# Kernel optimization log

Measured on AMD Instinct MI355X. Metric: run time of the kernel, lower is better.

Reference implementation:

```python
import jax, jax.numpy as jnp
import numpy as np

B, T, D = 2, 1024, 1024
H, HKV = 16, 8
HD = D // H           # 64
NREP = H // HKV       # 2
NLAYERS = 3
MAXKV = T * NLAYERS   # 3072
EPS = 1e-5


def setup_inputs() -> dict:
    key = jax.random.key(0)
    ks = jax.random.split(key, 8)
    # rotary tables over full accumulated-KV range
    inv_freq = 1.0 / (10000.0 ** (jnp.arange(0, HD, 2, dtype=jnp.float32) / HD))  # (HD/2,)
    t = jnp.arange(MAXKV, dtype=jnp.float32)
    freqs = jnp.outer(t, inv_freq)  # (MAXKV, HD/2)
    return {
        "x": jax.random.normal(ks[0], (B, T, D), jnp.float32),
        "cos": jnp.cos(freqs),
        "sin": jnp.sin(freqs),
        "q_w": jax.random.normal(ks[1], (NLAYERS, D, D), jnp.float32) * 0.02,
        "k_w": jax.random.normal(ks[2], (NLAYERS, D // NREP, D), jnp.float32) * 0.02,
        "v_w": jax.random.normal(ks[3], (NLAYERS, D // NREP, D), jnp.float32) * 0.02,
        "ln_w": jnp.ones((NLAYERS, D), jnp.float32),
        "lam": jax.random.normal(ks[4], (NLAYERS,), jnp.float32) * 0.1,
        "out_w": jax.random.normal(ks[5], (D, D), jnp.float32) * 0.02,
        "final_ln_w": jnp.ones((D,), jnp.float32),
        "alpha": jnp.ones((1,), jnp.float32),
    }


def rmsnorm(x, w):
    return x * jax.lax.rsqrt(jnp.mean(x * x, axis=-1, keepdims=True) + EPS) * w


def rope(x, cos, sin):
    # x: (B, L, h, HD); cos/sin: (MAXKV, HD/2); flash_attn non-interleaved rotary
    L = x.shape[1]
    c = jnp.concatenate([cos[:L], cos[:L]], axis=-1)[None, :, None, :]
    s = jnp.concatenate([sin[:L], sin[:L]], axis=-1)[None, :, None, :]
    x1, x2 = jnp.split(x, 2, axis=-1)
    rot = jnp.concatenate([-x2, x1], axis=-1)
    return x * c + rot * s


def reference(x, cos, sin, q_w, k_w, v_w, ln_w, lam, out_w, final_ln_w, alpha):
    scale = HD ** -0.5
    # lambda weights: layernorm over sigmoid of the 3 scalars (biased var, eps=1e-5)
    s = jax.nn.sigmoid(lam)
    lw = (s - s.mean()) * jax.lax.rsqrt(s.var() + EPS)
    qidx = jnp.arange(T)
    k_list, v_list = [], []
    acc = jnp.zeros_like(x)
    for i in range(NLAYERS):
        q = (x @ q_w[i].T).reshape(B, T, H, HD)
        k = (x @ k_w[i].T).reshape(B, T, HKV, HD)
        v = (x @ v_w[i].T).reshape(B, T, HKV, HD)
        k_list.append(k)
        v_list.append(v)
        K = jnp.concatenate(k_list, axis=1)  # (B, L, HKV, HD), L=(i+1)*T
        V = jnp.concatenate(v_list, axis=1)
        L = K.shape[1]
        qr = rope(q, cos, sin)
        Kr = rope(K, cos, sin)  # whole buffer re-rotated each layer, as in original
        Kr = jnp.repeat(Kr, NREP, axis=2)  # GQA expand
        Vr = jnp.repeat(V, NREP, axis=2)
        scores = jnp.einsum('bqhd,bkhd->bhqk', qr, Kr) * scale
        # flash_attn causal=True with kv_len > q_len aligns bottom-right
        mask = jnp.arange(L)[None, :] <= (qidx + (L - T))[:, None]
        scores = jnp.where(mask[None, None], scores, -jnp.inf)
        attn = jax.nn.softmax(scores, axis=-1)
        o = jnp.einsum('bhqk,bkhd->bqhd', attn, Vr).reshape(B, T, D)
        acc = acc + rmsnorm(o, ln_w[i]) * lw[i]
    out = rmsnorm(acc + alpha * x, final_ln_w)
    return out @ out_w.T
```

## Files before the change

### kernel.cpp

```cpp
#include <hip/hip_runtime.h>
#include <type_traits>
#include <utility>

typedef unsigned short u16;
typedef unsigned int u32;
typedef short short8 __attribute__((ext_vector_type(8)));
typedef short s16x4 __attribute__((ext_vector_type(4)));
typedef __bf16 bf16x8 __attribute__((ext_vector_type(8)));
typedef float floatx4 __attribute__((ext_vector_type(4)));

template <typename V, typename = void> struct MfmaTakes : std::false_type {};
template <typename V>
struct MfmaTakes<V, std::void_t<decltype(__builtin_amdgcn_mfma_f32_16x16x32_bf16(
    std::declval<V>(), std::declval<V>(), std::declval<floatx4>(), 0, 0, 0))>>
    : std::true_type {};

template <typename V>
__device__ __forceinline__ floatx4 mfma_impl(V a, V b, floatx4 c, std::true_type) {
  return __builtin_amdgcn_mfma_f32_16x16x32_bf16(a, b, c, 0, 0, 0);
}
template <typename V>
__device__ __forceinline__ floatx4 mfma_impl(V a, V b, floatx4 c, std::false_type) {
  return __builtin_amdgcn_mfma_f32_16x16x32_bf16(
      __builtin_bit_cast(bf16x8, a), __builtin_bit_cast(bf16x8, b), c, 0, 0, 0);
}
__device__ __forceinline__ floatx4 MFMA16(short8 a, short8 b, floatx4 c) {
  return mfma_impl<short8>(a, b, c, MfmaTakes<short8>{});
}

__device__ __forceinline__ floatx4 MFMAK16(s16x4 a, s16x4 b, floatx4 c) {
  return __builtin_amdgcn_mfma_f32_16x16x16bf16_1k(a, b, c, 0, 0, 0);
}

#if defined(__has_builtin)
#if __has_builtin(__builtin_amdgcn_exp2f)
#define EXP2(x) __builtin_amdgcn_exp2f(x)
#else
#define EXP2(x) exp2f(x)
#endif
#else
#define EXP2(x) exp2f(x)
#endif

__device__ __forceinline__ u16 f2bf(float f) {
  union { float f; unsigned u; } x; x.f = f;
  unsigned r = (x.u + 0x7fffu + ((x.u >> 16) & 1u)) >> 16;
  return (u16)r;
}
__device__ __forceinline__ float bf2f(u16 v) {
  union { unsigned u; float f; } x; x.u = ((unsigned)v) << 16; return x.f;
}
__device__ __forceinline__ u32 packbf(float lo, float hi) {
  return (__float_as_uint(hi) & 0xffff0000u) | (__float_as_uint(lo) >> 16);
}
__device__ __forceinline__ u32 pack2bf(float lo, float hi) {
  return ((u32)f2bf(hi) << 16) | (u32)f2bf(lo);
}

#if defined(__has_builtin)
#if __has_builtin(__builtin_amdgcn_global_load_lds)
#define HAS_GLLDS 1
#endif
#endif
__device__ __forceinline__ void stage16(const u16* g, u16* lbase, int lane) {
#ifdef HAS_GLLDS
  __builtin_amdgcn_global_load_lds(
      (__attribute__((address_space(1))) void*)(g),
      (__attribute__((address_space(3))) void*)(lbase), 16, 0, 0);
#else
  *(uint4*)(lbase + lane * 8) = *(const uint4*)g;
#endif
}

#define QSCALE 0.18033688011112042f

__global__ __launch_bounds__(256) void prep_kernel(
    const float* __restrict__ x, const float* __restrict__ qw,
    const float* __restrict__ kw, const float* __restrict__ vw,
    const float* __restrict__ outw, const float* __restrict__ lam,
    u16* __restrict__ xb, u16* __restrict__ wcat, u16* __restrict__ outwb,
    float* __restrict__ lwbuf) {
  size_t gid = (size_t)blockIdx.x * 256 + threadIdx.x;
  if (gid == 0) {
    float s0 = 1.f / (1.f + expf(-lam[0]));
    float s1 = 1.f / (1.f + expf(-lam[1]));
    float s2 = 1.f / (1.f + expf(-lam[2]));
    float mean = (s0 + s1 + s2) * (1.f / 3.f);
    float d0 = s0 - mean, d1 = s1 - mean, d2 = s2 - mean;
    float var = (d0 * d0 + d1 * d1 + d2 * d2) * (1.f / 3.f);
    float r = rsqrtf(var + 1e-5f);
    lwbuf[0] = d0 * r; lwbuf[1] = d1 * r; lwbuf[2] = d2 * r;
  }
  if (gid < 524288) {
    float4 v = ((const float4*)x)[gid];
    ushort4 o; o.x = f2bf(v.x); o.y = f2bf(v.y); o.z = f2bf(v.z); o.w = f2bf(v.w);
    ((ushort4*)xb)[gid] = o;
    return;
  }
  size_t g2 = gid - 524288;
  if (g2 < 1572864) {
    int col4 = (int)(g2 & 255);
    int n = (int)(g2 >> 8);
    int layer = n >> 11, r = n & 2047;
    const float* srcrow;
    if (r < 1024) srcrow = qw + ((size_t)(layer * 1024 + r) << 10);
    else if (r < 1536) srcrow = kw + ((size_t)(layer * 512 + (r - 1024)) << 10);
    else srcrow = vw + ((size_t)(layer * 512 + (r - 1536)) << 10);
    float4 v = ((const float4*)srcrow)[col4];
    ushort4 o; o.x = f2bf(v.x); o.y = f2bf(v.y); o.z = f2bf(v.z); o.w = f2bf(v.w);
    ((ushort4*)wcat)[g2] = o;
    return;
  }
  size_t g3 = g2 - 1572864;
  if (g3 < 262144) {
    float4 v = ((const float4*)outw)[g3];
    ushort4 o; o.x = f2bf(v.x); o.y = f2bf(v.y); o.z = f2bf(v.z); o.w = f2bf(v.w);
    ((ushort4*)outwb)[g3] = o;
  }
}

__global__ __launch_bounds__(256) void gemm_qkv(
    const u16* __restrict__ A, const u16* __restrict__ Bw,
    const float* __restrict__ cosb, const float* __restrict__ sinb,
    u16* __restrict__ qr, u16* __restrict__ kr, u16* __restrict__ vt) {
  __shared__ u16 As[128][64];
  __shared__ u16 Bs[128][64];
  const unsigned flat = blockIdx.x;
  const int bm = (flat >> 3) & 15;
  const int bn = ((flat >> 7) << 3) + (flat & 7);
  const int tid = threadIdx.x;
  const int wave = tid >> 6, lane = tid & 63;
  const int quad = lane >> 4, l16 = lane & 15;
  const int wm = wave & 1, wn = wave >> 1;
  const int srow = lane >> 3, skc = (lane & 7) * 8;
  floatx4 acc[4][4];
#pragma unroll
  for (int i = 0; i < 4; i++)
#pragma unroll
    for (int j = 0; j < 4; j++) { acc[i][j][0] = 0.f; acc[i][j][1] = 0.f; acc[i][j][2] = 0.f; acc[i][j][3] = 0.f; }
  const u16* Abase = A + (size_t)(bm * 128) * 1024;
  const u16* Bbase = Bw + (size_t)(bn * 128) * 1024;
  for (int k0 = 0; k0 < 1024; k0 += 64) {
    __syncthreads();
#pragma unroll
    for (int i = 0; i < 4; i++) {
      int ch = wave * 4 + i;
      stage16(Abase + (size_t)(ch * 8 + srow) * 1024 + k0 + skc, &As[ch * 8][0], lane);
      stage16(Bbase + (size_t)(ch * 8 + srow) * 1024 + k0 + skc, &Bs[ch * 8][0], lane);
    }
    __syncthreads();
#pragma unroll
    for (int kf = 0; kf < 2; kf++) {
      short8 af[4], bf[4];
#pragma unroll
      for (int mi = 0; mi < 4; mi++)
        af[mi] = *(const short8*)(&As[wm * 64 + mi * 16 + l16][kf * 32 + quad * 8]);
#pragma unroll
      for (int ni = 0; ni < 4; ni++)
        bf[ni] = *(const short8*)(&Bs[wn * 64 + ni * 16 + l16][kf * 32 + quad * 8]);
#pragma unroll
      for (int mi = 0; mi < 4; mi++)
#pragma unroll
        for (int ni = 0; ni < 4; ni++)
          acc[mi][ni] = MFMA16(af[mi], bf[ni], acc[mi][ni]);
    }
  }
  const int f0 = bn * 128 + wn * 64;
  const int lay = f0 >> 11;
  const int r0 = f0 & 2047;
  const int mrow0 = bm * 128 + wm * 64;
  if (r0 < 1024) {
    const int h = r0 >> 6;
#pragma unroll
    for (int mi = 0; mi < 4; mi++)
#pragma unroll
      for (int rr = 0; rr < 4; rr++) {
        int m = mrow0 + mi * 16 + quad * 4 + rr;
        int b = m >> 10, t = m & 1023;
        const float* cp = cosb + (size_t)t * 32;
        const float* sp = sinb + (size_t)t * 32;
        float c0 = cp[l16], s0 = sp[l16];
        float c1 = cp[16 + l16], s1 = sp[16 + l16];
        float x10 = acc[mi][0][rr], x20 = acc[mi][2][rr];
        float x11 = acc[mi][1][rr], x21 = acc[mi][3][rr];
        u16* row = qr + ((((size_t)lay * 2 + b) * 16 + h) * 1024 + t) * 64;
        row[l16]      = f2bf((x10 * c0 - x20 * s0) * QSCALE);
        row[16 + l16] = f2bf((x11 * c1 - x21 * s1) * QSCALE);
        row[32 + l16] = f2bf((x20 * c0 + x10 * s0) * QSCALE);
        row[48 + l16] = f2bf((x21 * c1 + x11 * s1) * QSCALE);
      }
  } else if (r0 < 1536) {
    const int hk = (r0 - 1024) >> 6;
#pragma unroll
    for (int mi = 0; mi < 4; mi++)
#pragma unroll
      for (int rr = 0; rr < 4; rr++) {
        int m = mrow0 + mi * 16 + quad * 4 + rr;
        int b = m >> 10, t = m & 1023;
        int pos = lay * 1024 + t;
        const float* cp = cosb + (size_t)pos * 32;
        const float* sp = sinb + (size_t)pos * 32;
        float c0 = cp[l16], s0 = sp[l16];
        float c1 = cp[16 + l16], s1 = sp[16 + l16];
        float x10 = acc[mi][0][rr], x20 = acc[mi][2][rr];
        float x11 = acc[mi][1][rr], x21 = acc[mi][3][rr];
        u16* row = kr + (((size_t)(b * 8 + hk)) * 3072 + pos) * 64;
        row[l16]      = f2bf(x10 * c0 - x20 * s0);
        row[16 + l16] = f2bf(x11 * c1 - x21 * s1);
        row[32 + l16] = f2bf(x20 * c0 + x10 * s0);
        row[48 + l16] = f2bf(x21 * c1 + x11 * s1);
      }
  } else {
    const int hv = (r0 - 1536) >> 6;
#pragma unroll
    for (int mi = 0; mi < 4; mi++) {
      int m0 = mrow0 + mi * 16 + quad * 4;
      int b = m0 >> 10;
      int pos0 = lay * 1024 + (m0 & 1023);
      u16* colbase = vt + ((size_t)(b * 8 + hv) * 64) * 3072 + pos0;
#pragma unroll
      for (int ni = 0; ni < 4; ni++) {
        int d = ni * 16 + l16;
        uint2 st;
        st.x = pack2bf(acc[mi][ni][0], acc[mi][ni][1]);
        st.y = pack2bf(acc[mi][ni][2], acc[mi][ni][3]);
        *(uint2*)(colbase + (size_t)d * 3072) = st;
      }
    }
  }
}

__global__ __launch_bounds__(256) void gemm_bt(
    const u16* __restrict__ A, const u16* __restrict__ Bw,
    float* __restrict__ C, int N, int K) {
  __shared__ u16 As[64][72];
  __shared__ u16 Bs[64][72];
  const int bm = blockIdx.x, bn = blockIdx.y;
  const int tid = threadIdx.x;
  const int wave = tid >> 6, lane = tid & 63;
  const int quad = lane >> 4, l16 = lane & 15;
  const int lr = tid >> 2, lc = (tid & 3) << 4;
  floatx4 acc[4];
#pragma unroll
  for (int i = 0; i < 4; i++) { acc[i][0] = 0.f; acc[i][1] = 0.f; acc[i][2] = 0.f; acc[i][3] = 0.f; }
  const u16* Arow = A + (size_t)(bm * 64 + lr) * K;
  const u16* Brow = Bw + (size_t)(bn * 64 + lr) * K;
  for (int k0 = 0; k0 < K; k0 += 64) {
    __syncthreads();
    *(uint4*)(&As[lr][lc])     = *(const uint4*)(Arow + k0 + lc);
    *(uint4*)(&As[lr][lc + 8]) = *(const uint4*)(Arow + k0 + lc + 8);
    *(uint4*)(&Bs[lr][lc])     = *(const uint4*)(Brow + k0 + lc);
    *(uint4*)(&Bs[lr][lc + 8]) = *(const uint4*)(Brow + k0 + lc + 8);
    __syncthreads();
    const int mrow = wave * 16 + l16;
    short8 a0 = *(const short8*)(&As[mrow][quad * 8]);
    short8 a1 = *(const short8*)(&As[mrow][32 + quad * 8]);
#pragma unroll
    for (int ns = 0; ns < 4; ns++) {
      short8 b0 = *(const short8*)(&Bs[ns * 16 + l16][quad * 8]);
      short8 b1 = *(const short8*)(&Bs[ns * 16 + l16][32 + quad * 8]);
      acc[ns] = MFMA16(a0, b0, acc[ns]);
      acc[ns] = MFMA16(a1, b1, acc[ns]);
    }
  }
#pragma unroll
  for (int ns = 0; ns < 4; ns++)
#pragma unroll
    for (int r = 0; r < 4; r++) {
      int row = bm * 64 + wave * 16 + quad * 4 + r;
      int col = bn * 64 + ns * 16 + l16;
      C[(size_t)row * N + col] = acc[ns][r];
    }
}

__global__ __launch_bounds__(256) void attn_v7(
    const u16* __restrict__ qr, const u16* __restrict__ kr,
    const u16* __restrict__ vt, u16* __restrict__ obS,
    float* __restrict__ lbufp) {
  __shared__ __align__(16) u16 Kt[2][32][72];
  __shared__ __align__(16) u16 Vtt[2][64][40];
  __shared__ __align__(16) u16 Pw[4][16][40];
  const unsigned flat = blockIdx.x;
  const int xcd = (int)(flat & 7);
  const int m = (int)(flat >> 3);
  const int qtile = m / 24;
  const int gidx = m - qtile * 24;
  const int bhz = gidx * 8 + xcd;
  const int z = bhz >> 5;
  const int bh = bhz & 31;
  const int lay = (z == 5) ? 0 : ((z == 0 || z == 4) ? 1 : 2);
  const int n = lay * 32 + qtile * 4 + 4;
  int kt0, kt1;
  if (lay == 0) { kt0 = 0; kt1 = n; }
  else if (lay == 1) { int hf = n >> 1; kt0 = (z == 0) ? 0 : hf; kt1 = (z == 0) ? hf : n; }
  else {
    int t1 = n / 3, t2 = (2 * n) / 3;
    kt0 = (z == 1) ? 0 : ((z == 2) ? t1 : t2);
    kt1 = (z == 1) ? t1 : ((z == 2) ? t2 : n);
  }
  const int maskkt = lay * 32 + qtile * 4;
  const int b = bh >> 4, h = bh & 15, hk = h >> 1;
  const int tid = threadIdx.x, wave = tid >> 6, lane = tid & 63;
  const int quad = lane >> 4, l16 = lane & 15;
  const int qeffbase = lay * 1024 + qtile * 128 + wave * 32;
  const u16* qpb = qr + ((((size_t)lay * 2 + b) * 16 + h) * 1024
                         + qtile * 128 + wave * 32 + l16) * 64 + quad * 8;
  short8 qf[2][2];
  qf[0][0] = *(const short8*)(qpb);
  qf[0][1] = *(const short8*)(qpb + 32);
  qf[1][0] = *(const short8*)(qpb + 1024);
  qf[1][1] = *(const short8*)(qpb + 1056);
  const s16x4 ones4 = {16256, 16256, 16256, 16256};
  floatx4 oacc[2][4];
#pragma unroll
  for (int nt = 0; nt < 2; nt++)
#pragma unroll
    for (int dt = 0; dt < 4; dt++) { oacc[nt][dt][0] = 0.f; oacc[nt][dt][1] = 0.f; oacc[nt][dt][2] = 0.f; oacc[nt][dt][3] = 0.f; }
  floatx4 lacc[2];
  lacc[0][0] = 0.f; lacc[0][1] = 0.f; lacc[0][2] = 0.f; lacc[0][3] = 0.f;
  lacc[1] = lacc[0];
  const int ksr = tid >> 3, ksc = (tid & 7) * 8;
  const int vdr = tid >> 2, vdc = (tid & 3) * 8;
  const u16* kp = kr + ((size_t)(b * 8 + hk) * 3072 + kt0 * 32 + ksr) * 64 + ksc;
  const u16* vp = vt + ((size_t)(b * 8 + hk) * 64 + vdr) * 3072 + kt0 * 32 + vdc;
  uint4 kA = *(const uint4*)kp;
  uint4 vA = *(const uint4*)vp;
  *(uint4*)(&Kt[0][ksr][ksc])  = kA;
  *(uint4*)(&Vtt[0][vdr][vdc]) = vA;
  kp += 2048; vp += 32;
  if (kt0 + 1 < kt1) { kA = *(const uint4*)kp; vA = *(const uint4*)vp; }
  for (int kt = kt0; kt < kt1; kt++) {
    const int p = (kt - kt0) & 1;
    __syncthreads();
    if (kt + 1 < kt1) {
      *(uint4*)(&Kt[p ^ 1][ksr][ksc])  = kA;
      *(uint4*)(&Vtt[p ^ 1][vdr][vdc]) = vA;
      kp += 2048; vp += 32;
      if (kt + 2 < kt1) { kA = *(const uint4*)kp; vA = *(const uint4*)vp; }
    }
    const bool needmask = (kt >= maskkt);
    uint2 pk[2][2];
#pragma unroll
    for (int mt = 0; mt < 2; mt++) {
      short8 kfa = *(const short8*)(&Kt[p][mt * 16 + l16][quad * 8]);
      short8 kfb = *(const short8*)(&Kt[p][mt * 16 + l16][32 + quad * 8]);
      const int keyb = kt * 32 + mt * 16 + quad * 4;
#pragma unroll
      for (int nt = 0; nt < 2; nt++) {
        floatx4 s; s[0] = 0.f; s[1] = 0.f; s[2] = 0.f; s[3] = 0.f;
        s = MFMA16(kfa, qf[nt][0], s);
        s = MFMA16(kfb, qf[nt][1], s);
        float p0 = EXP2(s[0]), p1 = EXP2(s[1]);
        float p2 = EXP2(s[2]), p3 = EXP2(s[3]);
        if (needmask) {
          int qpos = qeffbase + nt * 16 + l16;
          if (keyb + 0 > qpos) p0 = 0.f;
          if (keyb + 1 > qpos) p1 = 0.f;
          if (keyb + 2 > qpos) p2 = 0.f;
          if (keyb + 3 > qpos) p3 = 0.f;
        }
        pk[mt][nt].x = packbf(p0, p1);
        pk[mt][nt].y = packbf(p2, p3);
      }
    }
    s16x4 vfr[2][4];
#pragma unroll
    for (int dt = 0; dt < 4; dt++) {
      vfr[0][dt] = *(const s16x4*)(&Vtt[p][dt * 16 + l16][quad * 4]);
      vfr[1][dt] = *(const s16x4*)(&Vtt[p][dt * 16 + l16][16 + quad * 4]);
    }
#pragma unroll
    for (int nt = 0; nt < 2; nt++) {
      s16x4 p0f = __builtin_bit_cast(s16x4, pk[0][nt]);
      s16x4 p1f = __builtin_bit_cast(s16x4, pk[1][nt]);
      lacc[nt] = MFMAK16(ones4, p0f, lacc[nt]);
      lacc[nt] = MFMAK16(ones4, p1f, lacc[nt]);
#pragma unroll
      for (int dt = 0; dt < 4; dt++) {
        oacc[nt][dt] = MFMAK16(vfr[0][dt], p0f, oacc[nt][dt]);
        oacc[nt][dt] = MFMAK16(vfr[1][dt], p1f, oacc[nt][dt]);
      }
    }
  }
  float* Pf = (float*)(&Pw[wave][0][0]);
  const int tt = lane >> 2, dd = (lane & 3) << 2;
#pragma unroll
  for (int nt = 0; nt < 2; nt++) {
    int t = qtile * 128 + wave * 32 + nt * 16 + l16;
    if (quad == 0)
      lbufp[((size_t)z * 2048 + b * 1024 + t) * 16 + h] = lacc[nt][0];
    int t2 = qtile * 128 + wave * 32 + nt * 16 + tt;
    u16* orow = obS + ((size_t)(z * 2 + b) * 1024 + t2) * 1024 + h * 64 + dd;
#pragma unroll
    for (int dt = 0; dt < 4; dt++) {
      *(floatx4*)(&Pf[l16 * 20 + quad * 4]) = oacc[nt][dt];
      floatx4 val = *(const floatx4*)(&Pf[tt * 20 + dd]);
      uint2 st; st.x = pack2bf(val[0], val[1]); st.y = pack2bf(val[2], val[3]);
      *(uint2*)(orow + dt * 16) = st;
    }
  }
}

__device__ __forceinline__ float block_sum(float v, float* red) {
  v += __shfl_xor(v, 32); v += __shfl_xor(v, 16); v += __shfl_xor(v, 8);
  v += __shfl_xor(v, 4);  v += __shfl_xor(v, 2);  v += __shfl_xor(v, 1);
  __syncthreads();
  if ((threadIdx.x & 63) == 0) red[threadIdx.x >> 6] = v;
  __syncthreads();
  return red[0] + red[1] + red[2] + red[3];
}

__global__ __launch_bounds__(256) void fused_norm(
    const u16* __restrict__ obS, const float* __restrict__ lbufp,
    const float* __restrict__ x, const float* __restrict__ lnw,
    const float* __restrict__ lwbuf, const float* __restrict__ flnw,
    const float* __restrict__ alphap, u16* __restrict__ y) {
  __shared__ float red[4];
  const int row = blockIdx.x, tid = threadIdx.x;
  float a[4] = {0.f, 0.f, 0.f, 0.f};
  const int nsl[3] = {1, 2, 3};
  const int sl[3][3] = {{5, 0, 0}, {0, 4, 0}, {1, 2, 3}};
#pragma unroll
  for (int l = 0; l < 3; l++) {
    float o0 = 0.f, o1 = 0.f, o2 = 0.f, o3 = 0.f, ls = 0.f;
#pragma unroll
    for (int si = 0; si < 3; si++) {
      if (si >= nsl[l]) break;
      int z = sl[l][si];
      uint2 v = ((const uint2*)(obS + ((size_t)z * 2048 + row) * 1024))[tid];
      o0 += bf2f((u16)(v.x & 0xffff)); o1 += bf2f((u16)(v.x >> 16));
      o2 += bf2f((u16)(v.y & 0xffff)); o3 += bf2f((u16)(v.y >> 16));
      ls += lbufp[((size_t)z * 2048 + row) * 16 + (tid >> 4)];
    }
    float linv = 1.f / ls;
    float v0 = o0 * linv, v1 = o1 * linv, v2 = o2 * linv, v3 = o3 * linv;
    float ss = v0 * v0 + v1 * v1 + v2 * v2 + v3 * v3;
    ss = block_sum(ss, red);
    float rstd = rsqrtf(ss * (1.f / 1024.f) + 1e-5f);
    float lw = lwbuf[l];
    float4 w = ((const float4*)(lnw + (size_t)l * 1024))[tid];
    a[0] += v0 * rstd * w.x * lw;
    a[1] += v1 * rstd * w.y * lw;
    a[2] += v2 * rstd * w.z * lw;
    a[3] += v3 * rstd * w.w * lw;
  }
  const float aa = alphap[0];
  float4 xv = ((const float4*)(x + (size_t)row * 1024))[tid];
  float v0 = a[0] + aa * xv.x, v1 = a[1] + aa * xv.y;
  float v2 = a[2] + aa * xv.z, v3 = a[3] + aa * xv.w;
  float ss = v0 * v0 + v1 * v1 + v2 * v2 + v3 * v3;
  ss = block_sum(ss, red);
  float rstd = rsqrtf(ss * (1.f / 1024.f) + 1e-5f);
  float4 fw = ((const float4*)flnw)[tid];
  ushort4 o;
  o.x = f2bf(v0 * rstd * fw.x); o.y = f2bf(v1 * rstd * fw.y);
  o.z = f2bf(v2 * rstd * fw.z); o.w = f2bf(v3 * rstd * fw.w);
  ((ushort4*)(y + (size_t)row * 1024))[tid] = o;
}

extern "C" void kernel_launch(void* const* d_in, const int* in_sizes, int n_in,
                              void* d_out, int out_size, void* d_ws, size_t ws_size,
                              hipStream_t stream) {
  const float* x     = (const float*)d_in[0];
  const float* cosb  = (const float*)d_in[1];
  const float* sinb  = (const float*)d_in[2];
  const float* qw    = (const float*)d_in[3];
  const float* kw    = (const float*)d_in[4];
  const float* vw    = (const float*)d_in[5];
  const float* lnw   = (const float*)d_in[6];
  const float* lam   = (const float*)d_in[7];
  const float* outw  = (const float*)d_in[8];
  const float* flnw  = (const float*)d_in[9];
  const float* alphap= (const float*)d_in[10];
  float* out = (float*)d_out;
  char* ws = (char*)d_ws;
  u16*   xb    = (u16*)  (ws + 0);
  u16*   wcat  = (u16*)  (ws + 4194304);
  u16*   obS   = (u16*)  (ws + 0);
  u16*   outwb = (u16*)  (ws + 25165824);
  float* lwbuf = (float*)(ws + 27262976);
  u16*   qr    = (u16*)  (ws + 27264000);
  u16*   kr    = (u16*)  (ws + 39846912);
  u16*   vt    = (u16*)  (ws + 46138368);
  float* lbufp = (float*)(ws + 52429824);
  u16*   yb    = (u16*)  (ws + 53216256);

  prep_kernel<<<9216, 256, 0, stream>>>(x, qw, kw, vw, outw, lam, xb, wcat, outwb, lwbuf);
  gemm_qkv<<<768, 256, 0, stream>>>(xb, wcat, cosb, sinb, qr, kr, vt);
  attn_v7<<<1536, 256, 0, stream>>>(qr, kr, vt, obS, lbufp);
  fused_norm<<<2048, 256, 0, stream>>>(obS, lbufp, x, lnw, lwbuf, flnw, alphap, yb);
  gemm_bt<<<dim3(32, 16), 256, 0, stream>>>(yb, outwb, out, 1024, 1024);
}
```

Baseline: 250.3 us.

## Share K/V tiles across both GQA query heads in 512-thread attention blocks

The attention kernel now runs 512-thread blocks in which two groups of four waves handle the two query heads that share one KV head. Each K/V tile is loaded from global memory once and staged in shared memory for both heads, which halves K/V global traffic and shared-memory fill work per head. Half the threads load K and half load V, so each thread does one global load per tile instead of two. In exchange, blocks are larger with fewer in flight, and a new barrier is needed before shared memory is reused for the output transpose.

Result: no change. 248.6 us (-0.7%).

```diff
diff --git a/kernel.cpp b/kernel.cpp
--- a/kernel.cpp
+++ b/kernel.cpp
@@ -273,21 +273,22 @@
     }
 }
 
-__global__ __launch_bounds__(256) void attn_v7(
+__global__ __launch_bounds__(512) void attn_v8(
     const u16* __restrict__ qr, const u16* __restrict__ kr,
     const u16* __restrict__ vt, u16* __restrict__ obS,
     float* __restrict__ lbufp) {
-  __shared__ __align__(16) u16 Kt[2][32][72];
-  __shared__ __align__(16) u16 Vtt[2][64][40];
-  __shared__ __align__(16) u16 Pw[4][16][40];
+  __shared__ __align__(16) u16 smem[9728];
+  u16* KtB = smem;
+  u16* VtB = smem + 4608;
   const unsigned flat = blockIdx.x;
   const int xcd = (int)(flat & 7);
   const int m = (int)(flat >> 3);
-  const int qtile = m / 24;
-  const int gidx = m - qtile * 24;
-  const int bhz = gidx * 8 + xcd;
-  const int z = bhz >> 5;
-  const int bh = bhz & 31;
+  const int qtile = m / 12;
+  const int g = m - qtile * 12;
+  const int pid = g * 8 + xcd;
+  const int z = pid >> 4;
+  const int rb = pid & 15;
+  const int b = rb >> 3, j = rb & 7;
   const int lay = (z == 5) ? 0 : ((z == 0 || z == 4) ? 1 : 2);
   const int n = lay * 32 + qtile * 4 + 4;
   int kt0, kt1;
@@ -299,12 +300,13 @@
     kt1 = (z == 1) ? t1 : ((z == 2) ? t2 : n);
   }
   const int maskkt = lay * 32 + qtile * 4;
-  const int b = bh >> 4, h = bh & 15, hk = h >> 1;
   const int tid = threadIdx.x, wave = tid >> 6, lane = tid & 63;
   const int quad = lane >> 4, l16 = lane & 15;
-  const int qeffbase = lay * 1024 + qtile * 128 + wave * 32;
+  const int hw = wave >> 2, wq = wave & 3;
+  const int h = j * 2 + hw;
+  const int qeffbase = lay * 1024 + qtile * 128 + wq * 32;
   const u16* qpb = qr + ((((size_t)lay * 2 + b) * 16 + h) * 1024
-                         + qtile * 128 + wave * 32 + l16) * 64 + quad * 8;
+                         + qtile * 128 + wq * 32 + l16) * 64 + quad * 8;
   short8 qf[2][2];
   qf[0][0] = *(const short8*)(qpb);
   qf[0][1] = *(const short8*)(qpb + 32);
@@ -319,31 +321,36 @@
   floatx4 lacc[2];
   lacc[0][0] = 0.f; lacc[0][1] = 0.f; lacc[0][2] = 0.f; lacc[0][3] = 0.f;
   lacc[1] = lacc[0];
-  const int ksr = tid >> 3, ksc = (tid & 7) * 8;
-  const int vdr = tid >> 2, vdc = (tid & 3) * 8;
-  const u16* kp = kr + ((size_t)(b * 8 + hk) * 3072 + kt0 * 32 + ksr) * 64 + ksc;
-  const u16* vp = vt + ((size_t)(b * 8 + hk) * 64 + vdr) * 3072 + kt0 * 32 + vdc;
-  uint4 kA = *(const uint4*)kp;
-  uint4 vA = *(const uint4*)vp;
-  *(uint4*)(&Kt[0][ksr][ksc])  = kA;
-  *(uint4*)(&Vtt[0][vdr][vdc]) = vA;
-  kp += 2048; vp += 32;
-  if (kt0 + 1 < kt1) { kA = *(const uint4*)kp; vA = *(const uint4*)vp; }
+  const bool isK = (tid < 256);
+  const int t2i = tid & 255;
+  const int ksr = t2i >> 3, ksc = (t2i & 7) * 8;
+  const int vdr = t2i >> 2, vdc = (t2i & 3) * 8;
+  const u16* gp = isK
+      ? kr + ((size_t)(b * 8 + j) * 3072 + kt0 * 32 + ksr) * 64 + ksc
+      : vt + ((size_t)(b * 8 + j) * 64 + vdr) * 3072 + kt0 * 32 + vdc;
+  const size_t gstep = isK ? 2048 : 32;
+  u16* ld0 = isK ? &KtB[ksr * 72 + ksc] : &VtB[vdr * 40 + vdc];
+  u16* ld1 = isK ? &KtB[2304 + ksr * 72 + ksc] : &VtB[2560 + vdr * 40 + vdc];
+  uint4 gA = *(const uint4*)gp;
+  *(uint4*)ld0 = gA;
+  gp += gstep;
+  if (kt0 + 1 < kt1) gA = *(const uint4*)gp;
   for (int kt = kt0; kt < kt1; kt++) {
     const int p = (kt - kt0) & 1;
     __syncthreads();
     if (kt + 1 < kt1) {
-      *(uint4*)(&Kt[p ^ 1][ksr][ksc])  = kA;
-      *(uint4*)(&Vtt[p ^ 1][vdr][vdc]) = vA;
-      kp += 2048; vp += 32;
-      if (kt + 2 < kt1) { kA = *(const uint4*)kp; vA = *(const uint4*)vp; }
+      *(uint4*)(p ? ld0 : ld1) = gA;
+      gp += gstep;
+      if (kt + 2 < kt1) gA = *(const uint4*)gp;
     }
     const bool needmask = (kt >= maskkt);
+    const u16* Ktp = &KtB[p * 2304];
+    const u16* Vtp = &VtB[p * 2560];
     uint2 pk[2][2];
 #pragma unroll
     for (int mt = 0; mt < 2; mt++) {
-      short8 kfa = *(const short8*)(&Kt[p][mt * 16 + l16][quad * 8]);
-      short8 kfb = *(const short8*)(&Kt[p][mt * 16 + l16][32 + quad * 8]);
+      short8 kfa = *(const short8*)(&Ktp[(mt * 16 + l16) * 72 + quad * 8]);
+      short8 kfb = *(const short8*)(&Ktp[(mt * 16 + l16) * 72 + 32 + quad * 8]);
       const int keyb = kt * 32 + mt * 16 + quad * 4;
 #pragma unroll
       for (int nt = 0; nt < 2; nt++) {
@@ -366,8 +373,8 @@
     s16x4 vfr[2][4];
 #pragma unroll
     for (int dt = 0; dt < 4; dt++) {
-      vfr[0][dt] = *(const s16x4*)(&Vtt[p][dt * 16 + l16][quad * 4]);
-      vfr[1][dt] = *(const s16x4*)(&Vtt[p][dt * 16 + l16][16 + quad * 4]);
+      vfr[0][dt] = *(const s16x4*)(&Vtp[(dt * 16 + l16) * 40 + quad * 4]);
+      vfr[1][dt] = *(const s16x4*)(&Vtp[(dt * 16 + l16) * 40 + 16 + quad * 4]);
     }
 #pragma unroll
     for (int nt = 0; nt < 2; nt++) {
@@ -382,14 +389,15 @@
       }
     }
   }
-  float* Pf = (float*)(&Pw[wave][0][0]);
+  __syncthreads();
+  float* Pf = (float*)smem + wave * 320;
   const int tt = lane >> 2, dd = (lane & 3) << 2;
 #pragma unroll
   for (int nt = 0; nt < 2; nt++) {
-    int t = qtile * 128 + wave * 32 + nt * 16 + l16;
+    int t = qtile * 128 + wq * 32 + nt * 16 + l16;
     if (quad == 0)
       lbufp[((size_t)z * 2048 + b * 1024 + t) * 16 + h] = lacc[nt][0];
-    int t2 = qtile * 128 + wave * 32 + nt * 16 + tt;
+    int t2 = qtile * 128 + wq * 32 + nt * 16 + tt;
     u16* orow = obS + ((size_t)(z * 2 + b) * 1024 + t2) * 1024 + h * 64 + dd;
 #pragma unroll
     for (int dt = 0; dt < 4; dt++) {
@@ -487,7 +495,7 @@
 
   prep_kernel<<<9216, 256, 0, stream>>>(x, qw, kw, vw, outw, lam, xb, wcat, outwb, lwbuf);
   gemm_qkv<<<768, 256, 0, stream>>>(xb, wcat, cosb, sinb, qr, kr, vt);
-  attn_v7<<<1536, 256, 0, stream>>>(qr, kr, vt, obS, lbufp);
+  attn_v8<<<768, 512, 0, stream>>>(qr, kr, vt, obS, lbufp);
   fused_norm<<<2048, 256, 0, stream>>>(obS, lbufp, x, lnw, lwbuf, flnw, alphap, yb);
   gemm_bt<<<dim3(32, 16), 256, 0, stream>>>(yb, outwb, out, 1024, 1024);
 }
```

## Drop LDS staging in attention, load K/V fragments directly with per-wave causal trimming

Applied to the files above, without the earlier changes.

The attention kernel now launches 128-thread blocks with two waves, each owning 64 query rows instead of 32. It reads K and V fragments straight from global memory into registers with a one-step K prefetch, replacing the double-buffered LDS tiles and their per-iteration barriers. Each wave stops at its own causal boundary (kt1w), so it skips key tiles that are fully masked for its rows. Query tiles are also issued in reverse order so the longest blocks start first. The cost is more global/L2 traffic, because the two waves and the sibling heads no longer share staged K/V, plus higher register pressure from the doubled accumulators.

New measurement: 306.7 us. +22.6%, slower.

```diff
diff --git a/kernel.cpp b/kernel.cpp
--- a/kernel.cpp
+++ b/kernel.cpp
@@ -273,21 +273,20 @@
     }
 }
 
-__global__ __launch_bounds__(256) void attn_v7(
+__global__ __launch_bounds__(128) void attn_v10(
     const u16* __restrict__ qr, const u16* __restrict__ kr,
     const u16* __restrict__ vt, u16* __restrict__ obS,
     float* __restrict__ lbufp) {
-  __shared__ __align__(16) u16 Kt[2][32][72];
-  __shared__ __align__(16) u16 Vtt[2][64][40];
-  __shared__ __align__(16) u16 Pw[4][16][40];
+  __shared__ __align__(16) float Pw[2][320];
   const unsigned flat = blockIdx.x;
   const int xcd = (int)(flat & 7);
   const int m = (int)(flat >> 3);
-  const int qtile = m / 24;
-  const int gidx = m - qtile * 24;
-  const int bhz = gidx * 8 + xcd;
-  const int z = bhz >> 5;
-  const int bh = bhz & 31;
+  const int qtile = 7 - m / 24;
+  const int g = m % 24;
+  const int ph = g * 8 + xcd;
+  const int z = ph >> 5;
+  const int bh = ph & 31;
+  const int b = bh >> 4, h = bh & 15, hk = h >> 1;
   const int lay = (z == 5) ? 0 : ((z == 0 || z == 4) ? 1 : 2);
   const int n = lay * 32 + qtile * 4 + 4;
   int kt0, kt1;
@@ -298,58 +297,67 @@
     kt0 = (z == 1) ? 0 : ((z == 2) ? t1 : t2);
     kt1 = (z == 1) ? t1 : ((z == 2) ? t2 : n);
   }
-  const int maskkt = lay * 32 + qtile * 4;
-  const int b = bh >> 4, h = bh & 15, hk = h >> 1;
   const int tid = threadIdx.x, wave = tid >> 6, lane = tid & 63;
   const int quad = lane >> 4, l16 = lane & 15;
-  const int qeffbase = lay * 1024 + qtile * 128 + wave * 32;
+  const int wq = wave;
+  const int qeffbase = lay * 1024 + qtile * 128 + wq * 64;
+  const int maskkt = lay * 32 + qtile * 4 + wq * 2;
+  const int kt1w = min(kt1, maskkt + 2);
   const u16* qpb = qr + ((((size_t)lay * 2 + b) * 16 + h) * 1024
-                         + qtile * 128 + wave * 32 + l16) * 64 + quad * 8;
-  short8 qf[2][2];
-  qf[0][0] = *(const short8*)(qpb);
-  qf[0][1] = *(const short8*)(qpb + 32);
-  qf[1][0] = *(const short8*)(qpb + 1024);
-  qf[1][1] = *(const short8*)(qpb + 1056);
+                         + qtile * 128 + wq * 64 + l16) * 64 + quad * 8;
+  short8 qf[4][2];
+#pragma unroll
+  for (int nt = 0; nt < 4; nt++) {
+    qf[nt][0] = *(const short8*)(qpb + nt * 1024);
+    qf[nt][1] = *(const short8*)(qpb + nt * 1024 + 32);
+  }
   const s16x4 ones4 = {16256, 16256, 16256, 16256};
-  floatx4 oacc[2][4];
-#pragma unroll
-  for (int nt = 0; nt < 2; nt++)
-#pragma unroll
-    for (int dt = 0; dt < 4; dt++) { oacc[nt][dt][0] = 0.f; oacc[nt][dt][1] = 0.f; oacc[nt][dt][2] = 0.f; oacc[nt][dt][3] = 0.f; }
-  floatx4 lacc[2];
-  lacc[0][0] = 0.f; lacc[0][1] = 0.f; lacc[0][2] = 0.f; lacc[0][3] = 0.f;
-  lacc[1] = lacc[0];
-  const int ksr = tid >> 3, ksc = (tid & 7) * 8;
-  const int vdr = tid >> 2, vdc = (tid & 3) * 8;
-  const u16* kp = kr + ((size_t)(b * 8 + hk) * 3072 + kt0 * 32 + ksr) * 64 + ksc;
-  const u16* vp = vt + ((size_t)(b * 8 + hk) * 64 + vdr) * 3072 + kt0 * 32 + vdc;
-  uint4 kA = *(const uint4*)kp;
-  uint4 vA = *(const uint4*)vp;
-  *(uint4*)(&Kt[0][ksr][ksc])  = kA;
-  *(uint4*)(&Vtt[0][vdr][vdc]) = vA;
-  kp += 2048; vp += 32;
-  if (kt0 + 1 < kt1) { kA = *(const uint4*)kp; vA = *(const uint4*)vp; }
-  for (int kt = kt0; kt < kt1; kt++) {
-    const int p = (kt - kt0) & 1;
-    __syncthreads();
-    if (kt + 1 < kt1) {
-      *(uint4*)(&Kt[p ^ 1][ksr][ksc])  = kA;
-      *(uint4*)(&Vtt[p ^ 1][vdr][vdc]) = vA;
-      kp += 2048; vp += 32;
-      if (kt + 2 < kt1) { kA = *(const uint4*)kp; vA = *(const uint4*)vp; }
-    }
+  floatx4 oacc[4][4];
+  floatx4 lacc[4];
+#pragma unroll
+  for (int nt = 0; nt < 4; nt++) {
+    lacc[nt][0] = 0.f; lacc[nt][1] = 0.f; lacc[nt][2] = 0.f; lacc[nt][3] = 0.f;
+#pragma unroll
+    for (int dt = 0; dt < 4; dt++) {
+      oacc[nt][dt][0] = 0.f; oacc[nt][dt][1] = 0.f;
+      oacc[nt][dt][2] = 0.f; oacc[nt][dt][3] = 0.f;
+    }
+  }
+  const size_t bhk = (size_t)(b * 8 + hk);
+  const u16* kb = kr + (bhk * 3072 + (size_t)kt0 * 32 + l16) * 64 + quad * 8;
+  const u16* vb = vt + (bhk * 64 + l16) * 3072 + (size_t)kt0 * 32 + quad * 4;
+  short8 kfa[2], kfb[2];
+  kfa[0] = *(const short8*)(kb);
+  kfb[0] = *(const short8*)(kb + 32);
+  kfa[1] = *(const short8*)(kb + 1024);
+  kfb[1] = *(const short8*)(kb + 1056);
+  for (int kt = kt0; kt < kt1w; ++kt) {
+    const bool pf = (kt + 1 < kt1w);
+    short8 nfa0, nfb0, nfa1, nfb1;
+    if (pf) {
+      kb += 2048;
+      nfa0 = *(const short8*)(kb);
+      nfb0 = *(const short8*)(kb + 32);
+      nfa1 = *(const short8*)(kb + 1024);
+      nfb1 = *(const short8*)(kb + 1056);
+    }
+    s16x4 v0[4], v1[4];
+#pragma unroll
+    for (int dt = 0; dt < 4; dt++) {
+      v0[dt] = *(const s16x4*)(vb + (size_t)dt * 49152);
+      v1[dt] = *(const s16x4*)(vb + (size_t)dt * 49152 + 16);
+    }
+    vb += 32;
     const bool needmask = (kt >= maskkt);
-    uint2 pk[2][2];
+    uint2 pk[2][4];
 #pragma unroll
     for (int mt = 0; mt < 2; mt++) {
-      short8 kfa = *(const short8*)(&Kt[p][mt * 16 + l16][quad * 8]);
-      short8 kfb = *(const short8*)(&Kt[p][mt * 16 + l16][32 + quad * 8]);
       const int keyb = kt * 32 + mt * 16 + quad * 4;
 #pragma unroll
-      for (int nt = 0; nt < 2; nt++) {
+      for (int nt = 0; nt < 4; nt++) {
         floatx4 s; s[0] = 0.f; s[1] = 0.f; s[2] = 0.f; s[3] = 0.f;
-        s = MFMA16(kfa, qf[nt][0], s);
-        s = MFMA16(kfb, qf[nt][1], s);
+        s = MFMA16(kfa[mt], qf[nt][0], s);
+        s = MFMA16(kfb[mt], qf[nt][1], s);
         float p0 = EXP2(s[0]), p1 = EXP2(s[1]);
         float p2 = EXP2(s[2]), p3 = EXP2(s[3]);
         if (needmask) {
@@ -363,33 +371,28 @@
         pk[mt][nt].y = packbf(p2, p3);
       }
     }
-    s16x4 vfr[2][4];
-#pragma unroll
-    for (int dt = 0; dt < 4; dt++) {
-      vfr[0][dt] = *(const s16x4*)(&Vtt[p][dt * 16 + l16][quad * 4]);
-      vfr[1][dt] = *(const s16x4*)(&Vtt[p][dt * 16 + l16][16 + quad * 4]);
-    }
-#pragma unroll
-    for (int nt = 0; nt < 2; nt++) {
+#pragma unroll
+    for (int nt = 0; nt < 4; nt++) {
       s16x4 p0f = __builtin_bit_cast(s16x4, pk[0][nt]);
       s16x4 p1f = __builtin_bit_cast(s16x4, pk[1][nt]);
       lacc[nt] = MFMAK16(ones4, p0f, lacc[nt]);
       lacc[nt] = MFMAK16(ones4, p1f, lacc[nt]);
 #pragma unroll
       for (int dt = 0; dt < 4; dt++) {
-        oacc[nt][dt] = MFMAK16(vfr[0][dt], p0f, oacc[nt][dt]);
-        oacc[nt][dt] = MFMAK16(vfr[1][dt], p1f, oacc[nt][dt]);
+        oacc[nt][dt] = MFMAK16(v0[dt], p0f, oacc[nt][dt]);
+        oacc[nt][dt] = MFMAK16(v1[dt], p1f, oacc[nt][dt]);
       }
     }
-  }
-  float* Pf = (float*)(&Pw[wave][0][0]);
+    if (pf) { kfa[0] = nfa0; kfb[0] = nfb0; kfa[1] = nfa1; kfb[1] = nfb1; }
+  }
+  float* Pf = &Pw[wave][0];
   const int tt = lane >> 2, dd = (lane & 3) << 2;
 #pragma unroll
-  for (int nt = 0; nt < 2; nt++) {
-    int t = qtile * 128 + wave * 32 + nt * 16 + l16;
+  for (int nt = 0; nt < 4; nt++) {
+    int t = qtile * 128 + wq * 64 + nt * 16 + l16;
     if (quad == 0)
       lbufp[((size_t)z * 2048 + b * 1024 + t) * 16 + h] = lacc[nt][0];
-    int t2 = qtile * 128 + wave * 32 + nt * 16 + tt;
+    int t2 = qtile * 128 + wq * 64 + nt * 16 + tt;
     u16* orow = obS + ((size_t)(z * 2 + b) * 1024 + t2) * 1024 + h * 64 + dd;
 #pragma unroll
     for (int dt = 0; dt < 4; dt++) {
@@ -487,7 +490,7 @@
 
   prep_kernel<<<9216, 256, 0, stream>>>(x, qw, kw, vw, outw, lam, xb, wcat, outwb, lwbuf);
   gemm_qkv<<<768, 256, 0, stream>>>(xb, wcat, cosb, sinb, qr, kr, vt);
-  attn_v7<<<1536, 256, 0, stream>>>(qr, kr, vt, obS, lbufp);
+  attn_v10<<<1536, 128, 0, stream>>>(qr, kr, vt, obS, lbufp);
   fused_norm<<<2048, 256, 0, stream>>>(obS, lbufp, x, lnw, lwbuf, flnw, alphap, yb);
   gemm_bt<<<dim3(32, 16), 256, 0, stream>>>(yb, outwb, out, 1024, 1024);
 }
```
